# Performance work log

Hardware: AMD Instinct MI355X
Metric: run time of the kernel (lower is better)

The kernel has to match this reference:

```python
import jax, jax.numpy as jnp
import numpy as np

EMBED_DIM = 1024
NUM_HEADS = 16
HEAD_DIM = EMBED_DIM // NUM_HEADS


def setup_inputs() -> dict:
    key = jax.random.key(0)
    k1, k2, k3, k4, k5 = jax.random.split(key, 5)
    B, T, C = 2, 2048, EMBED_DIM
    x = jax.random.normal(k1, (B, T, C), dtype=jnp.float32)
    # Linear params stored as (in, out) so y = x @ W + b
    s = 1.0 / np.sqrt(C)
    W_qkv = jax.random.uniform(k2, (C, 3 * C), minval=-s, maxval=s, dtype=jnp.float32)
    b_qkv = jax.random.uniform(k3, (3 * C,), minval=-s, maxval=s, dtype=jnp.float32)
    W_out = jax.random.uniform(k4, (C, C), minval=-s, maxval=s, dtype=jnp.float32)
    b_out = jax.random.uniform(k5, (C,), minval=-s, maxval=s, dtype=jnp.float32)
    return {"x": x, "W_qkv": W_qkv, "b_qkv": b_qkv, "W_out": W_out, "b_out": b_out}


def reference(x, W_qkv, b_qkv, W_out, b_out):
    B, T, C = x.shape
    H, D = NUM_HEADS, HEAD_DIM
    qkv = x @ W_qkv + b_qkv                       # [B, T, 3C]
    qkv = qkv.reshape(B, T, 3, H, D)
    q = qkv[:, :, 0].transpose(0, 2, 1, 3)        # [B, H, T, D]
    k = qkv[:, :, 1].transpose(0, 2, 1, 3)
    v = qkv[:, :, 2].transpose(0, 2, 1, 3)
    scores = jnp.einsum('bhqd,bhkd->bhqk', q, k) / jnp.sqrt(jnp.float32(D))
    causal = jnp.tril(jnp.ones((T, T), dtype=bool))
    scores = jnp.where(causal, scores, -jnp.inf)
    attn = jax.nn.softmax(scores, axis=-1)        # [B, H, T, T]
    out = jnp.einsum('bhqk,bhkd->bhqd', attn, v)  # [B, H, T, D]
    out = out.transpose(0, 2, 1, 3).reshape(B, T, C)
    out = out @ W_out + b_out
    return out
```

## Files before the change

### kernel.cpp

```cpp
#include <hip/hip_runtime.h>
#include <hip/hip_bf16.h>
#include <stdint.h>

typedef __bf16 bf16x8 __attribute__((ext_vector_type(8)));
typedef float  f32x4  __attribute__((ext_vector_type(4)));

typedef __attribute__((address_space(1))) void gas1_t;
typedef __attribute__((address_space(3))) void as3_t;

__device__ __forceinline__ void gload_lds16(const void* g, void* l) {
  __builtin_amdgcn_global_load_lds((gas1_t*)g, (as3_t*)l, 16, 0, 0);
}

__device__ __forceinline__ f32x4 zero4() { f32x4 z = {0.f, 0.f, 0.f, 0.f}; return z; }

__device__ __forceinline__ unsigned pack_bf16x2(float a, float b) {
  __bf16 ha = (__bf16)a, hb = (__bf16)b;
  unsigned short ua = *(unsigned short*)&ha, ub = *(unsigned short*)&hb;
  return (unsigned)ua | ((unsigned)ub << 16);
}

__global__ void cvt_f32_to_bf16(const float* __restrict__ in, __bf16* __restrict__ out, int n) {
  int i = (blockIdx.x * 256 + threadIdx.x) * 8;
  if (i >= n) return;
  const f32x4 v0 = *(const f32x4*)(in + i);
  const f32x4 v1 = *(const f32x4*)(in + i + 4);
  bf16x8 o;
#pragma unroll
  for (int j = 0; j < 4; ++j) { o[j] = (__bf16)v0[j]; o[j + 4] = (__bf16)v1[j]; }
  *(bf16x8*)(out + i) = o;
}

__global__ void transpose_cast(const float* __restrict__ W, __bf16* __restrict__ WT,
                               int K, int N) {
  __shared__ float tile[32][33];
  const int n0 = blockIdx.x * 32, k0 = blockIdx.y * 32;
  const int tx = threadIdx.x, ty = threadIdx.y;
  for (int i = ty; i < 32; i += 8) tile[i][tx] = W[(size_t)(k0 + i) * N + n0 + tx];
  __syncthreads();
  for (int i = ty; i < 32; i += 8) WT[(size_t)(n0 + i) * K + k0 + tx] = (__bf16)tile[tx][i];
}

template <int OUT_BF16, int A_F32>
__global__ __launch_bounds__(256) void gemm_bt(const void* __restrict__ Ap,
                                               const __bf16* __restrict__ BT,
                                               const float* __restrict__ bias,
                                               void* __restrict__ Cout,
                                               int M, int N, int K) {
  __shared__ __bf16 As[2][4096];
  __shared__ __bf16 Bs[2][4096];
  const int tid = threadIdx.x;
  const int lane = tid & 63, w = tid >> 6;
  const int wr = w >> 1, wc = w & 1;
  const int lgrp = lane >> 4, lcol = lane & 15;
  const int m0 = blockIdx.y * 128, n0 = blockIdx.x * 128;

  f32x4 acc[4][4];
#pragma unroll
  for (int m = 0; m < 4; ++m)
#pragma unroll
    for (int n = 0; n < 4; ++n) acc[m][n] = zero4();

  const int nk = K >> 5;

  auto stageB = [&](int buf, int k0) {
#pragma unroll
    for (int q = 0; q < 2; ++q) {
      const int c = q * 256 + w * 64 + lane;
      const int row = c >> 2, kc = (c & 3) * 8;
      const int ldsoff = (q * 256 + w * 64) * 16;
      gload_lds16(BT + (size_t)(n0 + row) * K + k0 + kc, (char*)&Bs[buf][0] + ldsoff);
    }
  };
  auto stageA = [&](int buf, int k0) {
    if (A_F32) {
      const float* A = (const float*)Ap;
      const int c0 = tid * 2;
      const int row = c0 >> 2, kc = (c0 & 3) * 8;
      const float* src = A + (size_t)(m0 + row) * K + k0 + kc;
      const f32x4 v0 = *(const f32x4*)(src);
      const f32x4 v1 = *(const f32x4*)(src + 4);
      const f32x4 v2 = *(const f32x4*)(src + 8);
      const f32x4 v3 = *(const f32x4*)(src + 12);
      bf16x8 o0, o1;
#pragma unroll
      for (int j = 0; j < 4; ++j) {
        o0[j] = (__bf16)v0[j]; o0[j + 4] = (__bf16)v1[j];
        o1[j] = (__bf16)v2[j]; o1[j + 4] = (__bf16)v3[j];
      }
      *(bf16x8*)((char*)&As[buf][0] + c0 * 16) = o0;
      *(bf16x8*)((char*)&As[buf][0] + c0 * 16 + 16) = o1;
    } else {
      const __bf16* A = (const __bf16*)Ap;
#pragma unroll
      for (int q = 0; q < 2; ++q) {
        const int c = q * 256 + w * 64 + lane;
        const int row = c >> 2, kc = (c & 3) * 8;
        const int ldsoff = (q * 256 + w * 64) * 16;
        gload_lds16(A + (size_t)(m0 + row) * K + k0 + kc, (char*)&As[buf][0] + ldsoff);
      }
    }
  };

  stageA(0, 0);
  stageB(0, 0);
  __syncthreads();
  int cur = 0;
  for (int t = 0; t < nk; ++t) {
    if (t + 1 < nk) { stageA(cur ^ 1, (t + 1) * 32); stageB(cur ^ 1, (t + 1) * 32); }
    bf16x8 af[4], bfr[4];
#pragma unroll
    for (int m = 0; m < 4; ++m)
      af[m] = *(const bf16x8*)&As[cur][(wr * 64 + m * 16 + lcol) * 32 + lgrp * 8];
#pragma unroll
    for (int n = 0; n < 4; ++n)
      bfr[n] = *(const bf16x8*)&Bs[cur][(wc * 64 + n * 16 + lcol) * 32 + lgrp * 8];
    __builtin_amdgcn_s_setprio(1);
#pragma unroll
    for (int m = 0; m < 4; ++m)
#pragma unroll
      for (int n = 0; n < 4; ++n)
        acc[m][n] = __builtin_amdgcn_mfma_f32_16x16x32_bf16(af[m], bfr[n], acc[m][n], 0, 0, 0);
    __builtin_amdgcn_s_setprio(0);
    __syncthreads();
    cur ^= 1;
  }

#pragma unroll
  for (int m = 0; m < 4; ++m) {
#pragma unroll
    for (int n = 0; n < 4; ++n) {
      const int col = n0 + wc * 64 + n * 16 + lcol;
      const float bv = bias[col];
#pragma unroll
      for (int r = 0; r < 4; ++r) {
        const int row = m0 + wr * 64 + m * 16 + lgrp * 4 + r;
        const float v = acc[m][n][r] + bv;
        if (OUT_BF16)
          ((__bf16*)Cout)[(size_t)row * N + col] = (__bf16)v;
        else
          ((float*)Cout)[(size_t)row * N + col] = v;
      }
    }
  }
}

__global__ __launch_bounds__(512) void attn_fused(const __bf16* __restrict__ qkv,
                                                  __bf16* __restrict__ attnb) {
  __shared__ __bf16 Kl[64][80];
  __shared__ __bf16 Vt[64][80];
  __shared__ __bf16 Pl[8][16][80];
  const int tid = threadIdx.x, lane = tid & 63, w = tid >> 6;
  const int wl = w & 3;
  const int lgrp = lane >> 4, lcol = lane & 15;
  const int bh = blockIdx.y;
  const int pair = (bh & 16) ? (15 - blockIdx.x) : blockIdx.x;
  const int b = bh >> 4, h = bh & 15;
  const __bf16* base = qkv + (size_t)b * 2048 * 3072;

  const int qt = (w < 4) ? (31 - pair) : pair;
  const int qb = qt * 64;
  const int my_need = qt + 1;
  const int loop_len = 32 - pair;

  const int kvr = tid >> 3;
  const int d00 = (tid & 7) * 8;
  const int vcol = ((((kvr >> 3) ^ (tid & 7)) << 3) | (kvr & 7));
  const __bf16* kvbase = base + 1024 + h * 64 + d00;

  const int q_l = qb + wl * 16 + lcol;
  const __bf16* qptr = base + (size_t)q_l * 3072 + h * 64;
  const bf16x8 qf0 = *(const bf16x8*)(qptr + lgrp * 8);
  const bf16x8 qf1 = *(const bf16x8*)(qptr + 32 + lgrp * 8);

  float m1 = -1e30f, l1 = 0.f;
  f32x4 acc_o[4];
#pragma unroll
  for (int d = 0; d < 4; ++d) acc_o[d] = zero4();

  bf16x8 kf = *(const bf16x8*)(kvbase + (size_t)kvr * 3072);
  bf16x8 vf = *(const bf16x8*)(kvbase + (size_t)kvr * 3072 + 1024);

  for (int kvb = 0; kvb < loop_len; ++kvb) {
    const int kv0 = kvb * 64;
    __syncthreads();
    *(bf16x8*)&Kl[kvr][d00] = kf;
#pragma unroll
    for (int j = 0; j < 8; ++j) Vt[d00 + j][vcol] = vf[j];
    __syncthreads();
    if (kvb + 1 < loop_len) {
      const __bf16* p0 = kvbase + (size_t)(kv0 + 64 + kvr) * 3072;
      kf = *(const bf16x8*)p0;
      vf = *(const bf16x8*)(p0 + 1024);
    }

    if (kvb < my_need) {
      f32x4 accs[4];
      __builtin_amdgcn_s_setprio(1);
#pragma unroll
      for (int sub = 0; sub < 4; ++sub) {
        accs[sub] = zero4();
#pragma unroll
        for (int s = 0; s < 2; ++s) {
          const bf16x8 kb = *(const bf16x8*)&Kl[sub * 16 + lcol][s * 32 + lgrp * 8];
          accs[sub] = __builtin_amdgcn_mfma_f32_16x16x32_bf16(kb, s ? qf1 : qf0, accs[sub], 0, 0, 0);
        }
      }
      __builtin_amdgcn_s_setprio(0);

      float sv[4][4];
#pragma unroll
      for (int sub = 0; sub < 4; ++sub) {
        const int kvg = kv0 + sub * 16 + lgrp * 4;
#pragma unroll
        for (int r = 0; r < 4; ++r)
          sv[sub][r] = (kvg + r <= q_l) ? accs[sub][r] * 0.125f : -1e30f;
      }

      float mx[4];
#pragma unroll
      for (int sub = 0; sub < 4; ++sub)
        mx[sub] = fmaxf(fmaxf(sv[sub][0], sv[sub][1]), fmaxf(sv[sub][2], sv[sub][3]));
      float rm = fmaxf(fmaxf(mx[0], mx[1]), fmaxf(mx[2], mx[3]));
      rm = fmaxf(rm, __shfl_xor(rm, 16));
      rm = fmaxf(rm, __shfl_xor(rm, 32));
      const float nm = fmaxf(m1, rm);
      const float sf = __expf(m1 - nm);
      m1 = nm;

      float ps[4];
#pragma unroll
      for (int sub = 0; sub < 4; ++sub) {
#pragma unroll
        for (int r = 0; r < 4; ++r) {
          const float pv = __expf(sv[sub][r] - nm);
          sv[sub][r] = pv;
        }
        ps[sub] = (sv[sub][0] + sv[sub][1]) + (sv[sub][2] + sv[sub][3]);
      }
      float rs = (ps[0] + ps[1]) + (ps[2] + ps[3]);
      rs += __shfl_xor(rs, 16);
      rs += __shfl_xor(rs, 32);
      l1 = l1 * sf + rs;

#pragma unroll
      for (int d = 0; d < 4; ++d)
#pragma unroll
        for (int r = 0; r < 4; ++r) acc_o[d][r] *= sf;

#pragma unroll
      for (int sub = 0; sub < 4; ++sub) {
        uint2 pk;
        pk.x = pack_bf16x2(sv[sub][0], sv[sub][1]);
        pk.y = pack_bf16x2(sv[sub][2], sv[sub][3]);
        const int eoff = ((((sub * 2 + (lgrp >> 1)) ^ ((lcol >> 2) & 3)) << 3) | ((lgrp & 1) << 2));
        *(uint2*)&Pl[w][lcol][eoff] = pk;
      }
      asm volatile("s_waitcnt lgkmcnt(0)" ::: "memory");
      __builtin_amdgcn_sched_barrier(0);

      __builtin_amdgcn_s_setprio(1);
#pragma unroll
      for (int s = 0; s < 2; ++s) {
        const bf16x8 pf = *(const bf16x8*)&Pl[w][lcol][((4 * s + lgrp) ^ ((lcol >> 2) & 3)) * 8];
#pragma unroll
        for (int d = 0; d < 4; ++d) {
          const bf16x8 vfr = *(const bf16x8*)&Vt[d * 16 + lcol][((4 * s + lgrp) ^ ((2 * d + (lcol >> 3)) & 7)) * 8];
          acc_o[d] = __builtin_amdgcn_mfma_f32_16x16x32_bf16(vfr, pf, acc_o[d], 0, 0, 0);
        }
      }
      __builtin_amdgcn_s_setprio(0);
    }
  }

  const float inv_l = 1.0f / l1;
  __bf16* orow = attnb + (size_t)(b * 2048 + q_l) * 1024 + h * 64 + lgrp * 4;
#pragma unroll
  for (int d = 0; d < 4; ++d) {
    uint2 ov;
    ov.x = pack_bf16x2(acc_o[d][0] * inv_l, acc_o[d][1] * inv_l);
    ov.y = pack_bf16x2(acc_o[d][2] * inv_l, acc_o[d][3] * inv_l);
    *(uint2*)(orow + d * 16) = ov;
  }
}

extern "C" void kernel_launch(void* const* d_in, const int* in_sizes, int n_in,
                              void* d_out, int out_size, void* d_ws, size_t ws_size,
                              hipStream_t stream) {
  const float* x    = (const float*)d_in[0];
  const float* Wqkv = (const float*)d_in[1];
  const float* bqkv = (const float*)d_in[2];
  const float* Wout = (const float*)d_in[3];
  const float* bout = (const float*)d_in[4];
  float* out = (float*)d_out;

  char* ws = (char*)d_ws;
  __bf16* qkvb  = (__bf16*)(ws);
  __bf16* wqkvT = (__bf16*)(ws + (24u << 20));
  __bf16* xb    = (__bf16*)(ws + (30u << 20));
  __bf16* attnb = (__bf16*)(ws + (24u << 20));
  __bf16* woutT = (__bf16*)(ws);

  const bool big_ws = ws_size >= ((size_t)38 << 20);

  transpose_cast<<<dim3(3072 / 32, 1024 / 32), dim3(32, 8), 0, stream>>>(Wqkv, wqkvT, 1024, 3072);

  if (big_ws) {
    cvt_f32_to_bf16<<<dim3(4096 * 1024 / 2048), dim3(256), 0, stream>>>(x, xb, 4096 * 1024);
    gemm_bt<1, 0><<<dim3(3072 / 128, 4096 / 128), dim3(256), 0, stream>>>(
        (const void*)xb, wqkvT, bqkv, (void*)qkvb, 4096, 3072, 1024);
  } else {
    gemm_bt<1, 1><<<dim3(3072 / 128, 4096 / 128), dim3(256), 0, stream>>>(
        (const void*)x, wqkvT, bqkv, (void*)qkvb, 4096, 3072, 1024);
  }

  attn_fused<<<dim3(16, 2 * 16), dim3(512), 0, stream>>>(qkvb, attnb);

  transpose_cast<<<dim3(1024 / 32, 1024 / 32), dim3(32, 8), 0, stream>>>(Wout, woutT, 1024, 1024);

  gemm_bt<0, 0><<<dim3(1024 / 128, 4096 / 128), dim3(256), 0, stream>>>(
      (const void*)attnb, woutT, bout, (void*)out, 4096, 1024, 1024);
}
```

Measured before the change: 129.8 us.

## Restructure causal attention to 128-row query tiles with 128-key blocks

The attention kernel now gives each block 128 consecutive query rows (8 waves of 16) and walks the KV sequence in 128-key steps held as two 64-key LDS halves. This replaces the old pairing of a low and a high 64-row query tile. Causal masking is applied only on the diagonal block, and waves whose rows lie entirely before the second half skip that half. The 1/sqrt(D) scale is folded into the QKV GEMM epilogue for the Q columns, which removes the per-score multiply. The cost is uneven work across blocks, since the pairing-based load balancing is gone, plus more LDS per block and a higher launch-bounds occupancy hint.

```diff
diff --git a/kernel.cpp b/kernel.cpp
--- a/kernel.cpp
+++ b/kernel.cpp
@@ -41,7 +41,7 @@
   for (int i = ty; i < 32; i += 8) WT[(size_t)(n0 + i) * K + k0 + tx] = (__bf16)tile[tx][i];
 }
 
-template <int OUT_BF16, int A_F32>
+template <int OUT_BF16, int A_F32, int SCALE_Q>
 __global__ __launch_bounds__(256) void gemm_bt(const void* __restrict__ Ap,
                                                const __bf16* __restrict__ BT,
                                                const float* __restrict__ bias,
@@ -135,7 +135,8 @@
 #pragma unroll
       for (int r = 0; r < 4; ++r) {
         const int row = m0 + wr * 64 + m * 16 + lgrp * 4 + r;
-        const float v = acc[m][n][r] + bv;
+        float v = acc[m][n][r] + bv;
+        if (SCALE_Q && col < 1024) v *= 0.125f;
         if (OUT_BF16)
           ((__bf16*)Cout)[(size_t)row * N + col] = (__bf16)v;
         else
@@ -145,30 +146,28 @@
   }
 }
 
-__global__ __launch_bounds__(512) void attn_fused(const __bf16* __restrict__ qkv,
-                                                  __bf16* __restrict__ attnb) {
-  __shared__ __bf16 Kl[64][80];
-  __shared__ __bf16 Vt[64][80];
+__global__ __launch_bounds__(512, 4) void attn_fused(const __bf16* __restrict__ qkv,
+                                                     __bf16* __restrict__ attnb) {
+  __shared__ __bf16 Kl[2][64][80];
+  __shared__ __bf16 Vt[2][64][80];
   __shared__ __bf16 Pl[8][16][80];
   const int tid = threadIdx.x, lane = tid & 63, w = tid >> 6;
-  const int wl = w & 3;
   const int lgrp = lane >> 4, lcol = lane & 15;
   const int bh = blockIdx.y;
-  const int pair = (bh & 16) ? (15 - blockIdx.x) : blockIdx.x;
+  const int xp = (bh & 16) ? (15 - blockIdx.x) : blockIdx.x;
   const int b = bh >> 4, h = bh & 15;
   const __bf16* base = qkv + (size_t)b * 2048 * 3072;
 
-  const int qt = (w < 4) ? (31 - pair) : pair;
-  const int qb = qt * 64;
-  const int my_need = qt + 1;
-  const int loop_len = 32 - pair;
-
-  const int kvr = tid >> 3;
+  const int qb = xp * 128;
+  const int rw = qb + w * 16;
+  const int nkv = xp + 1;
+
+  const int krow = tid >> 3;
   const int d00 = (tid & 7) * 8;
-  const int vcol = ((((kvr >> 3) ^ (tid & 7)) << 3) | (kvr & 7));
-  const __bf16* kvbase = base + 1024 + h * 64 + d00;
-
-  const int q_l = qb + wl * 16 + lcol;
+  const int vcol = ((((krow >> 3) ^ (tid & 7)) << 3) | (krow & 7));
+  const __bf16* kvp = base + 1024 + h * 64 + d00;
+
+  const int q_l = rw + lcol;
   const __bf16* qptr = base + (size_t)q_l * 3072 + h * 64;
   const bf16x8 qf0 = *(const bf16x8*)(qptr + lgrp * 8);
   const bf16x8 qf1 = *(const bf16x8*)(qptr + 32 + lgrp * 8);
@@ -178,94 +177,139 @@
 #pragma unroll
   for (int d = 0; d < 4; ++d) acc_o[d] = zero4();
 
-  bf16x8 kf = *(const bf16x8*)(kvbase + (size_t)kvr * 3072);
-  bf16x8 vf = *(const bf16x8*)(kvbase + (size_t)kvr * 3072 + 1024);
-
-  for (int kvb = 0; kvb < loop_len; ++kvb) {
-    const int kv0 = kvb * 64;
+  bf16x8 kf0 = *(const bf16x8*)(kvp + (size_t)krow * 3072);
+  bf16x8 vf0 = *(const bf16x8*)(kvp + (size_t)krow * 3072 + 1024);
+  bf16x8 kf1 = *(const bf16x8*)(kvp + (size_t)(krow + 64) * 3072);
+  bf16x8 vf1 = *(const bf16x8*)(kvp + (size_t)(krow + 64) * 3072 + 1024);
+
+  for (int kvb = 0; kvb < nkv; ++kvb) {
+    const int kv0 = kvb * 128;
     __syncthreads();
-    *(bf16x8*)&Kl[kvr][d00] = kf;
-#pragma unroll
-    for (int j = 0; j < 8; ++j) Vt[d00 + j][vcol] = vf[j];
+    *(bf16x8*)&Kl[0][krow][d00] = kf0;
+    *(bf16x8*)&Kl[1][krow][d00] = kf1;
+#pragma unroll
+    for (int j = 0; j < 8; ++j) {
+      Vt[0][d00 + j][vcol] = vf0[j];
+      Vt[1][d00 + j][vcol] = vf1[j];
+    }
     __syncthreads();
-    if (kvb + 1 < loop_len) {
-      const __bf16* p0 = kvbase + (size_t)(kv0 + 64 + kvr) * 3072;
-      kf = *(const bf16x8*)p0;
-      vf = *(const bf16x8*)(p0 + 1024);
-    }
-
-    if (kvb < my_need) {
-      f32x4 accs[4];
-      __builtin_amdgcn_s_setprio(1);
+    if (kvb + 1 < nkv) {
+      const __bf16* p = kvp + (size_t)(kv0 + 128 + krow) * 3072;
+      kf0 = *(const bf16x8*)p;
+      vf0 = *(const bf16x8*)(p + 1024);
+      kf1 = *(const bf16x8*)(p + (size_t)64 * 3072);
+      vf1 = *(const bf16x8*)(p + (size_t)64 * 3072 + 1024);
+    }
+
+    const bool diag = (kvb == xp);
+    const bool skip1 = diag && (w < 4);
+
+    f32x4 accs[8];
+    __builtin_amdgcn_s_setprio(1);
+#pragma unroll
+    for (int sub = 0; sub < 4; ++sub) {
+      accs[sub] = zero4();
+#pragma unroll
+      for (int s = 0; s < 2; ++s) {
+        const bf16x8 kb = *(const bf16x8*)&Kl[0][sub * 16 + lcol][s * 32 + lgrp * 8];
+        accs[sub] = __builtin_amdgcn_mfma_f32_16x16x32_bf16(kb, s ? qf1 : qf0, accs[sub], 0, 0, 0);
+      }
+    }
+    if (!skip1) {
 #pragma unroll
       for (int sub = 0; sub < 4; ++sub) {
-        accs[sub] = zero4();
+        accs[4 + sub] = zero4();
 #pragma unroll
         for (int s = 0; s < 2; ++s) {
-          const bf16x8 kb = *(const bf16x8*)&Kl[sub * 16 + lcol][s * 32 + lgrp * 8];
-          accs[sub] = __builtin_amdgcn_mfma_f32_16x16x32_bf16(kb, s ? qf1 : qf0, accs[sub], 0, 0, 0);
+          const bf16x8 kb = *(const bf16x8*)&Kl[1][sub * 16 + lcol][s * 32 + lgrp * 8];
+          accs[4 + sub] = __builtin_amdgcn_mfma_f32_16x16x32_bf16(kb, s ? qf1 : qf0, accs[4 + sub], 0, 0, 0);
         }
       }
-      __builtin_amdgcn_s_setprio(0);
-
-      float sv[4][4];
-#pragma unroll
-      for (int sub = 0; sub < 4; ++sub) {
+    } else {
+#pragma unroll
+      for (int sub = 4; sub < 8; ++sub) accs[sub] = f32x4{-1e30f, -1e30f, -1e30f, -1e30f};
+    }
+    __builtin_amdgcn_s_setprio(0);
+
+    if (diag) {
+#pragma unroll
+      for (int sub = 0; sub < 8; ++sub) {
         const int kvg = kv0 + sub * 16 + lgrp * 4;
 #pragma unroll
         for (int r = 0; r < 4; ++r)
-          sv[sub][r] = (kvg + r <= q_l) ? accs[sub][r] * 0.125f : -1e30f;
-      }
-
-      float mx[4];
-#pragma unroll
-      for (int sub = 0; sub < 4; ++sub)
-        mx[sub] = fmaxf(fmaxf(sv[sub][0], sv[sub][1]), fmaxf(sv[sub][2], sv[sub][3]));
-      float rm = fmaxf(fmaxf(mx[0], mx[1]), fmaxf(mx[2], mx[3]));
-      rm = fmaxf(rm, __shfl_xor(rm, 16));
-      rm = fmaxf(rm, __shfl_xor(rm, 32));
-      const float nm = fmaxf(m1, rm);
-      const float sf = __expf(m1 - nm);
-      m1 = nm;
-
-      float ps[4];
-#pragma unroll
-      for (int sub = 0; sub < 4; ++sub) {
-#pragma unroll
-        for (int r = 0; r < 4; ++r) {
-          const float pv = __expf(sv[sub][r] - nm);
-          sv[sub][r] = pv;
-        }
-        ps[sub] = (sv[sub][0] + sv[sub][1]) + (sv[sub][2] + sv[sub][3]);
-      }
-      float rs = (ps[0] + ps[1]) + (ps[2] + ps[3]);
-      rs += __shfl_xor(rs, 16);
-      rs += __shfl_xor(rs, 32);
-      l1 = l1 * sf + rs;
-
-#pragma unroll
-      for (int d = 0; d < 4; ++d)
-#pragma unroll
-        for (int r = 0; r < 4; ++r) acc_o[d][r] *= sf;
-
+          if (kvg + r > q_l) accs[sub][r] = -1e30f;
+      }
+    }
+
+    float mx[8];
+#pragma unroll
+    for (int sub = 0; sub < 8; ++sub)
+      mx[sub] = fmaxf(fmaxf(accs[sub][0], accs[sub][1]), fmaxf(accs[sub][2], accs[sub][3]));
+    float rm = fmaxf(fmaxf(fmaxf(mx[0], mx[1]), fmaxf(mx[2], mx[3])),
+                     fmaxf(fmaxf(mx[4], mx[5]), fmaxf(mx[6], mx[7])));
+    rm = fmaxf(rm, __shfl_xor(rm, 16));
+    rm = fmaxf(rm, __shfl_xor(rm, 32));
+    const float nm = fmaxf(m1, rm);
+    const float sf = __expf(m1 - nm);
+    m1 = nm;
+
+    float ps[8];
+#pragma unroll
+    for (int sub = 0; sub < 8; ++sub) {
+#pragma unroll
+      for (int r = 0; r < 4; ++r) accs[sub][r] = __expf(accs[sub][r] - nm);
+      ps[sub] = (accs[sub][0] + accs[sub][1]) + (accs[sub][2] + accs[sub][3]);
+    }
+    float rs = ((ps[0] + ps[1]) + (ps[2] + ps[3])) + ((ps[4] + ps[5]) + (ps[6] + ps[7]));
+    rs += __shfl_xor(rs, 16);
+    rs += __shfl_xor(rs, 32);
+    l1 = l1 * sf + rs;
+
+#pragma unroll
+    for (int d = 0; d < 4; ++d)
+#pragma unroll
+      for (int r = 0; r < 4; ++r) acc_o[d][r] *= sf;
+
+#pragma unroll
+    for (int sub = 0; sub < 4; ++sub) {
+      uint2 pk;
+      pk.x = pack_bf16x2(accs[sub][0], accs[sub][1]);
+      pk.y = pack_bf16x2(accs[sub][2], accs[sub][3]);
+      const int eoff = ((((sub * 2 + (lgrp >> 1)) ^ ((lcol >> 2) & 3)) << 3) | ((lgrp & 1) << 2));
+      *(uint2*)&Pl[w][lcol][eoff] = pk;
+    }
+    asm volatile("s_waitcnt lgkmcnt(0)" ::: "memory");
+    __builtin_amdgcn_sched_barrier(0);
+    __builtin_amdgcn_s_setprio(1);
+#pragma unroll
+    for (int s = 0; s < 2; ++s) {
+      const bf16x8 pf = *(const bf16x8*)&Pl[w][lcol][((4 * s + lgrp) ^ ((lcol >> 2) & 3)) * 8];
+#pragma unroll
+      for (int d = 0; d < 4; ++d) {
+        const bf16x8 vfr = *(const bf16x8*)&Vt[0][d * 16 + lcol][((4 * s + lgrp) ^ ((2 * d + (lcol >> 3)) & 7)) * 8];
+        acc_o[d] = __builtin_amdgcn_mfma_f32_16x16x32_bf16(vfr, pf, acc_o[d], 0, 0, 0);
+      }
+    }
+    __builtin_amdgcn_s_setprio(0);
+
+    if (!skip1) {
 #pragma unroll
       for (int sub = 0; sub < 4; ++sub) {
         uint2 pk;
-        pk.x = pack_bf16x2(sv[sub][0], sv[sub][1]);
-        pk.y = pack_bf16x2(sv[sub][2], sv[sub][3]);
+        pk.x = pack_bf16x2(accs[4 + sub][0], accs[4 + sub][1]);
+        pk.y = pack_bf16x2(accs[4 + sub][2], accs[4 + sub][3]);
         const int eoff = ((((sub * 2 + (lgrp >> 1)) ^ ((lcol >> 2) & 3)) << 3) | ((lgrp & 1) << 2));
         *(uint2*)&Pl[w][lcol][eoff] = pk;
       }
       asm volatile("s_waitcnt lgkmcnt(0)" ::: "memory");
       __builtin_amdgcn_sched_barrier(0);
-
       __builtin_amdgcn_s_setprio(1);
 #pragma unroll
       for (int s = 0; s < 2; ++s) {
         const bf16x8 pf = *(const bf16x8*)&Pl[w][lcol][((4 * s + lgrp) ^ ((lcol >> 2) & 3)) * 8];
 #pragma unroll
         for (int d = 0; d < 4; ++d) {
-          const bf16x8 vfr = *(const bf16x8*)&Vt[d * 16 + lcol][((4 * s + lgrp) ^ ((2 * d + (lcol >> 3)) & 7)) * 8];
+          const bf16x8 vfr = *(const bf16x8*)&Vt[1][d * 16 + lcol][((4 * s + lgrp) ^ ((2 * d + (lcol >> 3)) & 7)) * 8];
           acc_o[d] = __builtin_amdgcn_mfma_f32_16x16x32_bf16(vfr, pf, acc_o[d], 0, 0, 0);
         }
       }
@@ -307,10 +351,10 @@
 
   if (big_ws) {
     cvt_f32_to_bf16<<<dim3(4096 * 1024 / 2048), dim3(256), 0, stream>>>(x, xb, 4096 * 1024);
-    gemm_bt<1, 0><<<dim3(3072 / 128, 4096 / 128), dim3(256), 0, stream>>>(
+    gemm_bt<1, 0, 1><<<dim3(3072 / 128, 4096 / 128), dim3(256), 0, stream>>>(
         (const void*)xb, wqkvT, bqkv, (void*)qkvb, 4096, 3072, 1024);
   } else {
-    gemm_bt<1, 1><<<dim3(3072 / 128, 4096 / 128), dim3(256), 0, stream>>>(
+    gemm_bt<1, 1, 1><<<dim3(3072 / 128, 4096 / 128), dim3(256), 0, stream>>>(
         (const void*)x, wqkvT, bqkv, (void*)qkvb, 4096, 3072, 1024);
   }
 
@@ -318,6 +362,6 @@
 
   transpose_cast<<<dim3(1024 / 32, 1024 / 32), dim3(32, 8), 0, stream>>>(Wout, woutT, 1024, 1024);
 
-  gemm_bt<0, 0><<<dim3(1024 / 128, 4096 / 128), dim3(256), 0, stream>>>(
+  gemm_bt<0, 0, 0><<<dim3(1024 / 128, 4096 / 128), dim3(256), 0, stream>>>(
       (const void*)attnb, woutT, bout, (void*)out, 4096, 1024, 1024);
 }
```

New measurement: 123.6 us. -4.7%, faster.
